# Performance work log

Hardware: AMD Instinct MI355X
Metric: run time of the kernel (lower is better)

Reference implementation:

```python
import jax, jax.numpy as jnp
import numpy as np

M, K, N = 32, 8192, 8192  # tokens, in_features, out_features
PACK = 8  # int4 nibbles per int32


def setup_inputs() -> dict:
    key = jax.random.key(0)
    k1, k2, k3, k4 = jax.random.split(key, 4)
    x = (jax.random.normal(k1, (M, K), dtype=jnp.float32)).astype(jnp.float16)
    # packed int4 weights: 8 signed nibbles per int32, [N, K//8]
    b_packed = jax.random.randint(k2, (N, K // PACK), 0, 2147483647, dtype=jnp.int32)
    # rowwise fp16 scales (meta), one per output row; small positive values
    scales = (jax.random.uniform(k3, (N,), dtype=jnp.float32) * 0.01 + 1e-4).astype(jnp.float16)
    bias = (jax.random.normal(k4, (N,), dtype=jnp.float32) * 0.01).astype(jnp.float16)
    return {"x": x, "b_packed": b_packed, "scales": scales, "bias": bias}


def _unpack_int4(b_packed):
    # b_packed: [N, K//8] int32 -> signed int4 values in [-8, 7], shape [N, K]
    shifts = (jnp.arange(PACK, dtype=jnp.int32) * 4)  # [8]
    nib = (b_packed[:, :, None] >> shifts) & 0xF       # [N, K//8, 8]
    q = jnp.where(nib >= 8, nib - 16, nib)             # two's-complement nibble
    return q.reshape(b_packed.shape[0], -1)            # [N, K]


def reference(x, b_packed, scales, bias):
    # Rowwise dequant: W[n, k] = q[n, k] * scale[n]  (fp16), then y = x @ W^T + bias
    q = _unpack_int4(b_packed).astype(jnp.float16)          # [N, K]
    W = q * scales[:, None]                                  # [N, K] fp16
    y = jnp.einsum('mk,nk->mn', x, W,
                   preferred_element_type=jnp.float32).astype(jnp.float16)
    y = y + bias.astype(y.dtype)
    return y
```

## Files before the change

kernel.cpp:

```cpp
#include <hip/hip_runtime.h>
#include <cstdint>

#define M_DIM 32
#define K_DIM 8192
#define N_DIM 8192

typedef _Float16 f16x8 __attribute__((ext_vector_type(8)));
typedef float    f32x4 __attribute__((ext_vector_type(4)));

__device__ __forceinline__ f16x8 dq8(uint32_t w) {
  f16x8 r;
#pragma unroll
  for (int j = 0; j < 8; ++j) {
    int q = ((int)(w << (28 - 4 * j))) >> 28;
    r[j] = (_Float16)q;
  }
  return r;
}

__device__ __forceinline__ uint32_t u4e(uint4 v, int t) {
  return (t == 0) ? v.x : (t == 1) ? v.y : (t == 2) ? v.z : v.w;
}

__global__ __launch_bounds__(256) void xprep_kernel(
    const float* __restrict__ x, uint4* __restrict__ xp) {
  const int T = blockIdx.x * 256 + threadIdx.x;
  const int m = T >> 10;
  const int g = T & 1023;
  const f32x4* p = (const f32x4*)(x + (size_t)m * K_DIM + (size_t)g * 8);
  f32x4 lo = p[0], hi = p[1];
  union { uint4 q; f16x8 v; } o;
#pragma unroll
  for (int j = 0; j < 4; ++j) {
    o.v[j]     = (_Float16)lo[j];
    o.v[j + 4] = (_Float16)hi[j];
  }
  xp[(size_t)g * 32 + m] = o.q;
}

__global__ __launch_bounds__(1024, 4) void qgemm_xp(
    const uint32_t* __restrict__ bq,
    const uint4*    __restrict__ xp,
    const float*    __restrict__ sc,
    const float*    __restrict__ bi,
    float*          __restrict__ out) {
  __shared__ float red[16][32][33];

  const int tid  = threadIdx.x;
  const int w    = tid >> 6;
  const int lane = tid & 63;
  const int l16  = lane & 15;
  const int quad = lane >> 4;
  const int n0   = blockIdx.x << 5;

  const uint4* bq4 = (const uint4*)bq;
  const uint4* bp0 = bq4 + (size_t)(n0 + l16) * 256 + (w << 4) + quad;
  const uint4* bp1 = bp0 + (size_t)16 * 256;
  const uint4* ap  = xp + (size_t)(((w << 6) + (quad << 2)) * 32 + l16);

  uint4 b0[4], b1[4];
#pragma unroll
  for (int c = 0; c < 4; ++c) { b0[c] = bp0[c * 4]; b1[c] = bp1[c * 4]; }

  uint4 a[8], an[8];
#pragma unroll
  for (int t = 0; t < 4; ++t) {
    a[t]     = ap[t * 32];
    a[4 + t] = ap[t * 32 + 16];
  }

  f32x4 acc00 = {0.f, 0.f, 0.f, 0.f};
  f32x4 acc01 = {0.f, 0.f, 0.f, 0.f};
  f32x4 acc10 = {0.f, 0.f, 0.f, 0.f};
  f32x4 acc11 = {0.f, 0.f, 0.f, 0.f};

#pragma unroll
  for (int c = 0; c < 4; ++c) {
    const int cn = (c + 1) & 3;
#pragma unroll
    for (int t = 0; t < 4; ++t) {
      an[t]     = ap[(cn * 16 + t) * 32];
      an[4 + t] = ap[(cn * 16 + t) * 32 + 16];
    }
#pragma unroll
    for (int t = 0; t < 4; ++t) {
      f16x8 fb0 = dq8(u4e(b0[c], t));
      f16x8 fb1 = dq8(u4e(b1[c], t));
      f16x8 fa0 = __builtin_bit_cast(f16x8, a[t]);
      f16x8 fa1 = __builtin_bit_cast(f16x8, a[4 + t]);
      acc00 = __builtin_amdgcn_mfma_f32_16x16x32_f16(fa0, fb0, acc00, 0, 0, 0);
      acc01 = __builtin_amdgcn_mfma_f32_16x16x32_f16(fa1, fb0, acc01, 0, 0, 0);
      acc10 = __builtin_amdgcn_mfma_f32_16x16x32_f16(fa0, fb1, acc10, 0, 0, 0);
      acc11 = __builtin_amdgcn_mfma_f32_16x16x32_f16(fa1, fb1, acc11, 0, 0, 0);
    }
#pragma unroll
    for (int i = 0; i < 8; ++i) a[i] = an[i];
  }

#pragma unroll
  for (int r = 0; r < 4; ++r) {
    const int mr = (quad << 2) + r;
    red[w][l16][mr]           = acc00[r];
    red[w][l16][mr + 16]      = acc01[r];
    red[w][l16 + 16][mr]      = acc10[r];
    red[w][l16 + 16][mr + 16] = acc11[r];
  }

  __syncthreads();

  const int n = tid & 31;
  const int m = tid >> 5;
  float s = 0.f;
#pragma unroll
  for (int ww = 0; ww < 16; ++ww) s += red[ww][n][m];
  const int gn = n0 + n;
  out[(size_t)m * N_DIM + gn] = fmaf(s, sc[gn], bi[gn]);
}

__global__ __launch_bounds__(512) void qgemm_direct(
    const uint32_t* __restrict__ bq, const float* __restrict__ x,
    const float* __restrict__ sc, const float* __restrict__ bi,
    float* __restrict__ out) {
  __shared__ float red[8][32][40];

  const int tid  = threadIdx.x;
  const int w    = tid >> 6;
  const int lane = tid & 63;
  const int l16  = lane & 15;
  const int quad = lane >> 4;
  const int n0   = blockIdx.x << 5;

  const uint4* bq4 = (const uint4*)bq;
  const uint4* bp0 = bq4 + (size_t)(n0 + l16) * 256 + (w << 5) + quad;
  const uint4* bp1 = bp0 + (size_t)16 * 256;
  const float* ap0 = x + (size_t)l16 * K_DIM + (w << 10) + (quad << 5);
  const float* ap1 = ap0 + (size_t)16 * K_DIM;

  f32x4 acc00 = {0.f,0.f,0.f,0.f}, acc01 = {0.f,0.f,0.f,0.f};
  f32x4 acc10 = {0.f,0.f,0.f,0.f}, acc11 = {0.f,0.f,0.f,0.f};

#pragma unroll
  for (int c = 0; c < 8; ++c) {
    const uint4 wb0 = bp0[c * 4];
    const uint4 wb1 = bp1[c * 4];
#pragma unroll
    for (int t = 0; t < 4; ++t) {
      const float* a0 = ap0 + c * 128 + t * 8;
      const float* a1 = ap1 + c * 128 + t * 8;
      f32x4 l0 = *(const f32x4*)a0, h0 = *(const f32x4*)(a0 + 4);
      f32x4 l1 = *(const f32x4*)a1, h1 = *(const f32x4*)(a1 + 4);
      f16x8 fa0, fa1;
#pragma unroll
      for (int j = 0; j < 4; ++j) {
        fa0[j] = (_Float16)l0[j]; fa0[j+4] = (_Float16)h0[j];
        fa1[j] = (_Float16)l1[j]; fa1[j+4] = (_Float16)h1[j];
      }
      f16x8 fb0 = dq8(u4e(wb0, t));
      f16x8 fb1 = dq8(u4e(wb1, t));
      acc00 = __builtin_amdgcn_mfma_f32_16x16x32_f16(fa0, fb0, acc00, 0, 0, 0);
      acc01 = __builtin_amdgcn_mfma_f32_16x16x32_f16(fa1, fb0, acc01, 0, 0, 0);
      acc10 = __builtin_amdgcn_mfma_f32_16x16x32_f16(fa0, fb1, acc10, 0, 0, 0);
      acc11 = __builtin_amdgcn_mfma_f32_16x16x32_f16(fa1, fb1, acc11, 0, 0, 0);
    }
  }

#pragma unroll
  for (int r = 0; r < 4; ++r) {
    const int mr = (quad << 2) + r;
    red[w][l16][mr]           = acc00[r];
    red[w][l16][mr + 16]      = acc01[r];
    red[w][l16 + 16][mr]      = acc10[r];
    red[w][l16 + 16][mr + 16] = acc11[r];
  }
  __syncthreads();
  const int n  = tid & 31;
  const int mh = tid >> 5;
  float s0 = 0.f, s1 = 0.f;
#pragma unroll
  for (int ww = 0; ww < 8; ++ww) {
    s0 += red[ww][n][mh];
    s1 += red[ww][n][mh + 16];
  }
  const int gn = n0 + n;
  out[(size_t)mh * N_DIM + gn]        = fmaf(s0, sc[gn], bi[gn]);
  out[(size_t)(mh + 16) * N_DIM + gn] = fmaf(s1, sc[gn], bi[gn]);
}

extern "C" void kernel_launch(void* const* d_in, const int* in_sizes, int n_in,
                              void* d_out, int out_size, void* d_ws, size_t ws_size,
                              hipStream_t stream) {
  const float*    x  = (const float*)d_in[0];
  const uint32_t* bq = (const uint32_t*)d_in[1];
  const float*    sc = (const float*)d_in[2];
  const float*    bi = (const float*)d_in[3];
  float*          y  = (float*)d_out;

  const size_t XP_BYTES = (size_t)M_DIM * K_DIM * 2;
  if (ws_size >= XP_BYTES) {
    uint4* xp = (uint4*)d_ws;
    xprep_kernel<<<128, 256, 0, stream>>>(x, xp);
    qgemm_xp<<<N_DIM / 32, 1024, 0, stream>>>(bq, xp, sc, bi, y);
  } else {
    qgemm_direct<<<N_DIM / 32, 512, 0, stream>>>(bq, x, sc, bi, y);
  }
}
```

Before: 87.75 us.

## Use magic-number fp16 int4 dequant with interleaved K order and shallower x prefetch

Replaces the per-nibble shift and int-to-half conversion with a packed mask/XOR/subtract trick that turns two nibbles into two fp16 values per 32-bit op. The trick yields weights in an interleaved order (nibbles 0,4,1,5,...), so the x packing in both the prep kernel and the direct kernel is permuted to match. The A-operand prefetch is reduced from eight 16-byte registers per step to a one-step-ahead pair, lowering register pressure. Correctness depends on the x permutation exactly matching the dequant's nibble order, and the shallower prefetch may expose more load latency.

```diff
diff --git a/kernel.cpp b/kernel.cpp
--- a/kernel.cpp
+++ b/kernel.cpp
@@ -6,20 +6,25 @@
 #define N_DIM 8192
 
 typedef _Float16 f16x8 __attribute__((ext_vector_type(8)));
+typedef _Float16 f16x2 __attribute__((ext_vector_type(2)));
 typedef float    f32x4 __attribute__((ext_vector_type(4)));
-
-__device__ __forceinline__ f16x8 dq8(uint32_t w) {
-  f16x8 r;
-#pragma unroll
-  for (int j = 0; j < 8; ++j) {
-    int q = ((int)(w << (28 - 4 * j))) >> 28;
-    r[j] = (_Float16)q;
-  }
-  return r;
-}
 
 __device__ __forceinline__ uint32_t u4e(uint4 v, int t) {
   return (t == 0) ? v.x : (t == 1) ? v.y : (t == 2) ? v.z : v.w;
+}
+
+__device__ __forceinline__ f16x8 dq8(uint32_t w) {
+  union { uint32_t u[4]; f16x8 v; } r;
+  const uint32_t MASK  = 0x000F000Fu;
+  const uint32_t MAGIC = 0x64086408u;
+  const f16x2 magic = __builtin_bit_cast(f16x2, MAGIC);
+#pragma unroll
+  for (int s = 0; s < 4; ++s) {
+    uint32_t t = ((w >> (4 * s)) & MASK) ^ MAGIC;
+    f16x2 h = __builtin_bit_cast(f16x2, t) - magic;
+    r.u[s] = __builtin_bit_cast(uint32_t, h);
+  }
+  return r.v;
 }
 
 __global__ __launch_bounds__(256) void xprep_kernel(
@@ -31,9 +36,9 @@
   f32x4 lo = p[0], hi = p[1];
   union { uint4 q; f16x8 v; } o;
 #pragma unroll
-  for (int j = 0; j < 4; ++j) {
-    o.v[j]     = (_Float16)lo[j];
-    o.v[j + 4] = (_Float16)hi[j];
+  for (int s = 0; s < 4; ++s) {
+    o.v[2 * s]     = (_Float16)lo[s];
+    o.v[2 * s + 1] = (_Float16)hi[s];
   }
   xp[(size_t)g * 32 + m] = o.q;
 }
@@ -62,39 +67,30 @@
 #pragma unroll
   for (int c = 0; c < 4; ++c) { b0[c] = bp0[c * 4]; b1[c] = bp1[c * 4]; }
 
-  uint4 a[8], an[8];
-#pragma unroll
-  for (int t = 0; t < 4; ++t) {
-    a[t]     = ap[t * 32];
-    a[4 + t] = ap[t * 32 + 16];
-  }
-
   f32x4 acc00 = {0.f, 0.f, 0.f, 0.f};
   f32x4 acc01 = {0.f, 0.f, 0.f, 0.f};
   f32x4 acc10 = {0.f, 0.f, 0.f, 0.f};
   f32x4 acc11 = {0.f, 0.f, 0.f, 0.f};
 
+  uint4 a0c = ap[0], a1c = ap[16];
 #pragma unroll
-  for (int c = 0; c < 4; ++c) {
-    const int cn = (c + 1) & 3;
-#pragma unroll
-    for (int t = 0; t < 4; ++t) {
-      an[t]     = ap[(cn * 16 + t) * 32];
-      an[4 + t] = ap[(cn * 16 + t) * 32 + 16];
-    }
-#pragma unroll
-    for (int t = 0; t < 4; ++t) {
-      f16x8 fb0 = dq8(u4e(b0[c], t));
-      f16x8 fb1 = dq8(u4e(b1[c], t));
-      f16x8 fa0 = __builtin_bit_cast(f16x8, a[t]);
-      f16x8 fa1 = __builtin_bit_cast(f16x8, a[4 + t]);
-      acc00 = __builtin_amdgcn_mfma_f32_16x16x32_f16(fa0, fb0, acc00, 0, 0, 0);
-      acc01 = __builtin_amdgcn_mfma_f32_16x16x32_f16(fa1, fb0, acc01, 0, 0, 0);
-      acc10 = __builtin_amdgcn_mfma_f32_16x16x32_f16(fa0, fb1, acc10, 0, 0, 0);
-      acc11 = __builtin_amdgcn_mfma_f32_16x16x32_f16(fa1, fb1, acc11, 0, 0, 0);
-    }
-#pragma unroll
-    for (int i = 0; i < 8; ++i) a[i] = an[i];
+  for (int g = 0; g < 16; ++g) {
+    const int gn  = (g + 1) & 15;
+    const int off = (((gn >> 2) * 16) + (gn & 3)) * 32;
+    uint4 a0n = ap[off];
+    uint4 a1n = ap[off + 16];
+
+    const int c = g >> 2, t = g & 3;
+    f16x8 fb0 = dq8(u4e(b0[c], t));
+    f16x8 fb1 = dq8(u4e(b1[c], t));
+    f16x8 fa0 = __builtin_bit_cast(f16x8, a0c);
+    f16x8 fa1 = __builtin_bit_cast(f16x8, a1c);
+    acc00 = __builtin_amdgcn_mfma_f32_16x16x32_f16(fa0, fb0, acc00, 0, 0, 0);
+    acc01 = __builtin_amdgcn_mfma_f32_16x16x32_f16(fa1, fb0, acc01, 0, 0, 0);
+    acc10 = __builtin_amdgcn_mfma_f32_16x16x32_f16(fa0, fb1, acc10, 0, 0, 0);
+    acc11 = __builtin_amdgcn_mfma_f32_16x16x32_f16(fa1, fb1, acc11, 0, 0, 0);
+
+    a0c = a0n; a1c = a1n;
   }
 
 #pragma unroll
@@ -122,7 +118,6 @@
     const float* __restrict__ sc, const float* __restrict__ bi,
     float* __restrict__ out) {
   __shared__ float red[8][32][40];
-
   const int tid  = threadIdx.x;
   const int w    = tid >> 6;
   const int lane = tid & 63;
@@ -138,7 +133,6 @@
 
   f32x4 acc00 = {0.f,0.f,0.f,0.f}, acc01 = {0.f,0.f,0.f,0.f};
   f32x4 acc10 = {0.f,0.f,0.f,0.f}, acc11 = {0.f,0.f,0.f,0.f};
-
 #pragma unroll
   for (int c = 0; c < 8; ++c) {
     const uint4 wb0 = bp0[c * 4];
@@ -151,9 +145,9 @@
       f32x4 l1 = *(const f32x4*)a1, h1 = *(const f32x4*)(a1 + 4);
       f16x8 fa0, fa1;
 #pragma unroll
-      for (int j = 0; j < 4; ++j) {
-        fa0[j] = (_Float16)l0[j]; fa0[j+4] = (_Float16)h0[j];
-        fa1[j] = (_Float16)l1[j]; fa1[j+4] = (_Float16)h1[j];
+      for (int s = 0; s < 4; ++s) {
+        fa0[2*s] = (_Float16)l0[s]; fa0[2*s+1] = (_Float16)h0[s];
+        fa1[2*s] = (_Float16)l1[s]; fa1[2*s+1] = (_Float16)h1[s];
       }
       f16x8 fb0 = dq8(u4e(wb0, t));
       f16x8 fb1 = dq8(u4e(wb1, t));
@@ -163,7 +157,6 @@
       acc11 = __builtin_amdgcn_mfma_f32_16x16x32_f16(fa1, fb1, acc11, 0, 0, 0);
     }
   }
-
 #pragma unroll
   for (int r = 0; r < 4; ++r) {
     const int mr = (quad << 2) + r;
@@ -177,10 +170,7 @@
   const int mh = tid >> 5;
   float s0 = 0.f, s1 = 0.f;
 #pragma unroll
-  for (int ww = 0; ww < 8; ++ww) {
-    s0 += red[ww][n][mh];
-    s1 += red[ww][n][mh + 16];
-  }
+  for (int ww = 0; ww < 8; ++ww) { s0 += red[ww][n][mh]; s1 += red[ww][n][mh+16]; }
   const int gn = n0 + n;
   out[(size_t)mh * N_DIM + gn]        = fmaf(s0, sc[gn], bi[gn]);
   out[(size_t)(mh + 16) * N_DIM + gn] = fmaf(s1, sc[gn], bi[gn]);
```

Measured after the change: 87.39 us. No clear change (-0.4%).
